# Kernel optimization log

Hardware: AMD Instinct MI355X
Metric: run time of the kernel (lower is better)

The kernel has to match this reference:

```python
import jax, jax.numpy as jnp
import numpy as np

H = 4          # no_heads
C_HIDDEN = 32  # per-head hidden dim


def setup_inputs() -> dict:
    key = jax.random.key(0)
    ks = jax.random.split(key, 11)
    B, S, C = 1, 256, 128
    sc = 1.0 / np.sqrt(C).astype(np.float32)
    return {
        "q_x": jax.random.normal(ks[0], (B, S, S, C), jnp.float32),
        "kv_x": jax.random.normal(ks[1], (B, S, S, C), jnp.float32),
        "bias1": jax.random.normal(ks[2], (B, 1, H, S, S), jnp.float32),
        "bias2": jax.random.normal(ks[3], (B, S, 1, 1, S), jnp.float32),
        "wq": jax.random.normal(ks[4], (C, C), jnp.float32) * sc,
        "wk": jax.random.normal(ks[5], (C, C), jnp.float32) * sc,
        "wv": jax.random.normal(ks[6], (C, C), jnp.float32) * sc,
        "wg": jax.random.normal(ks[7], (C, C), jnp.float32) * sc,
        "bg": jax.random.normal(ks[8], (C,), jnp.float32) * 0.02,
        "wo": jax.random.normal(ks[9], (C, C), jnp.float32) * sc,
        "bo": jax.random.normal(ks[10], (C,), jnp.float32) * 0.02,
    }


def reference(q_x, kv_x, bias1, bias2, wq, wk, wv, wg, bg, wo, bo):
    # Linear projections (torch Linear semantics: x @ W^T), no bias on q/k/v.
    def split_heads(x):  # ... Q (H C) -> ... H Q C
        *lead, Q, _ = x.shape
        return jnp.moveaxis(x.reshape(*lead, Q, H, C_HIDDEN), -2, -3)

    q = split_heads(jnp.einsum('...qi,oi->...qo', q_x, wq)) / np.sqrt(C_HIDDEN)
    k = split_heads(jnp.einsum('...ki,oi->...ko', kv_x, wk))
    v = split_heads(jnp.einsum('...ki,oi->...ko', kv_x, wv))

    # scores: [B, S, H, Q, K]
    a = jnp.einsum('bshqd,bshkd->bshqk', q, k)
    a = a + bias1 + bias2
    a = jax.nn.softmax(a, axis=-1)
    o = jnp.einsum('bshqk,bshkd->bshqd', a, v)
    o = jnp.moveaxis(o, -3, -2)  # ... H Q C -> ... Q H C

    # sigmoid gating
    g = jax.nn.sigmoid(jnp.einsum('...qi,oi->...qo', q_x, wg) + bg)
    *lead, Q, _ = g.shape
    g = g.reshape(*lead, Q, H, C_HIDDEN)
    o = o * g

    o = o.reshape(*lead, Q, H * C_HIDDEN)
    return jnp.einsum('...qi,oi->...qo', o, wo) + bo
```

## Files before the change

kernel.cpp:

```cpp
#include <hip/hip_runtime.h>
#include <math.h>

typedef _Float16 f16;
typedef _Float16 h4 __attribute__((ext_vector_type(4)));
typedef _Float16 h8 __attribute__((ext_vector_type(8)));
typedef float f32x4 __attribute__((ext_vector_type(4)));

#define QSCALE 0.17677669529663689f

__global__ __launch_bounds__(256) void proj_mfma(
    const float* __restrict__ q_x, const float* __restrict__ kv_x,
    const float* __restrict__ wq, const float* __restrict__ wk,
    const float* __restrict__ wv, const float* __restrict__ wg,
    const float* __restrict__ bg,
    f16* __restrict__ qb, f16* __restrict__ kb,
    f16* __restrict__ vbT, f16* __restrict__ gb)
{
    __shared__ char lds[65536];
    char* xl = lds;
    char* wl = lds + 32768;
    const int t = threadIdx.x;
    const int lane = t & 63, wave = t >> 6;
    const int wr = wave >> 1, wc = wave & 1;
    const int lo = lane & 15, hi = lane >> 4;
    const int phase = blockIdx.y;
    const int row0 = blockIdx.x * 128;
    const float* xsrc = phase ? kv_x : q_x;

    #pragma unroll
    for (int j = 0; j < 16; ++j) {
        int f = t + 256 * j;
        int row = f >> 5, c4 = f & 31;
        float4 v = *(const float4*)(xsrc + (size_t)(row0 + row) * 128 + c4 * 4);
        h4 hv = {(f16)v.x, (f16)v.y, (f16)v.z, (f16)v.w};
        *(h4*)(xl + row * 256 + (((c4 >> 1) ^ (row & 7)) << 4) + ((c4 & 1) << 3)) = hv;
    }

    for (int sub = 0; sub < 2; ++sub) {
        const int pid = phase * 2 + sub;
        const float* w = (pid == 0) ? wq : (pid == 1) ? wg : (pid == 2) ? wk : wv;
        __syncthreads();
        #pragma unroll
        for (int j = 0; j < 16; ++j) {
            int f = t + 256 * j;
            int row = f >> 5, c4 = f & 31;
            float4 v = *(const float4*)(w + (size_t)row * 128 + c4 * 4);
            h4 hv = {(f16)v.x, (f16)v.y, (f16)v.z, (f16)v.w};
            *(h4*)(wl + row * 256 + (((c4 >> 1) ^ (row & 7)) << 4) + ((c4 & 1) << 3)) = hv;
        }
        __syncthreads();

        f32x4 acc[4][4];
        #pragma unroll
        for (int m = 0; m < 4; ++m)
            #pragma unroll
            for (int n = 0; n < 4; ++n) acc[m][n] = (f32x4){0.f, 0.f, 0.f, 0.f};

        #pragma unroll
        for (int kk = 0; kk < 4; ++kk) {
            const int swz = ((hi + 4 * kk) ^ (lo & 7)) << 4;
            h8 af[4], bf[4];
            #pragma unroll
            for (int m = 0; m < 4; ++m)
                af[m] = *(const h8*)(xl + (lo + 16 * m + 64 * wr) * 256 + swz);
            #pragma unroll
            for (int n = 0; n < 4; ++n)
                bf[n] = *(const h8*)(wl + (lo + 16 * n + 64 * wc) * 256 + swz);
            #pragma unroll
            for (int m = 0; m < 4; ++m)
                #pragma unroll
                for (int n = 0; n < 4; ++n)
                    acc[m][n] = __builtin_amdgcn_mfma_f32_16x16x32_f16(af[m], bf[n], acc[m][n], 0, 0, 0);
        }

        #pragma unroll
        for (int n = 0; n < 4; ++n) {
            const int col = 64 * wc + 16 * n + lo;
            const float bgv = (pid == 1) ? bg[col] : 0.f;
            #pragma unroll
            for (int m = 0; m < 4; ++m) {
                if (pid == 3) {
                    int rg = row0 + 64 * wr + 16 * m + 4 * hi;
                    int sidx = rg >> 8, key = rg & 255;
                    int hh = col >> 5, dh = col & 31;
                    h4 hv = {(f16)acc[m][n][0], (f16)acc[m][n][1],
                             (f16)acc[m][n][2], (f16)acc[m][n][3]};
                    *(h4*)(vbT + (((size_t)sidx * 4 + hh) * 32 + dh) * 256 + key) = hv;
                } else {
                    f16* dst = (pid == 0) ? qb : (pid == 1) ? gb : kb;
                    #pragma unroll
                    for (int r = 0; r < 4; ++r) {
                        int rg = row0 + 64 * wr + 16 * m + 4 * hi + r;
                        float v = acc[m][n][r];
                        if (pid == 0) v *= QSCALE;
                        else if (pid == 1) v = 1.f / (1.f + __expf(-(v + bgv)));
                        dst[(size_t)rg * 128 + col] = (f16)v;
                    }
                }
            }
        }
    }
}

__global__ __launch_bounds__(256) void attn_mfma(
    const f16* __restrict__ qb, const f16* __restrict__ kb,
    const f16* __restrict__ vbT, const f16* __restrict__ gb,
    const float* __restrict__ bias1, const float* __restrict__ bias2,
    f16* __restrict__ ob)
{
    __shared__ float b2s[256];
    __shared__ char plds[32768];
    const int x = blockIdx.x;
    const int h = x >> 2, qblk = x & 3;
    const int s = blockIdx.y;
    const int t = threadIdx.x, wave = t >> 6, lane = t & 63;
    const int lo = lane & 15, hi = lane >> 4;
    char* pw = plds + wave * 8192;
    const size_t rowbase = (size_t)s * 256;
    const int q0 = qblk * 64 + wave * 16;

    b2s[t] = bias2[s * 256 + t];
    __syncthreads();

    h8 qf = *(const h8*)(qb + (rowbase + q0 + lo) * 128 + h * 32 + 8 * hi);

    const float* b1 = bias1 + (size_t)h * 65536;
    f32x4 acc[16];
    #pragma unroll
    for (int nt = 0; nt < 16; ++nt) {
        float b2v = b2s[16 * nt + lo];
        #pragma unroll
        for (int r = 0; r < 4; ++r)
            acc[nt][r] = b1[(q0 + 4 * hi + r) * 256 + 16 * nt + lo] + b2v;
    }
    #pragma unroll
    for (int nt = 0; nt < 16; ++nt) {
        h8 kf = *(const h8*)(kb + (rowbase + 16 * nt + lo) * 128 + h * 32 + 8 * hi);
        acc[nt] = __builtin_amdgcn_mfma_f32_16x16x32_f16(qf, kf, acc[nt], 0, 0, 0);
    }

    float inv_l[4];
    #pragma unroll
    for (int r = 0; r < 4; ++r) {
        float mx = acc[0][r];
        #pragma unroll
        for (int nt = 1; nt < 16; ++nt) mx = fmaxf(mx, acc[nt][r]);
        #pragma unroll
        for (int w = 1; w < 16; w <<= 1) mx = fmaxf(mx, __shfl_xor(mx, w, 16));
        float sm = 0.f;
        #pragma unroll
        for (int nt = 0; nt < 16; ++nt) {
            float p = __expf(acc[nt][r] - mx);
            acc[nt][r] = p;
            sm += p;
        }
        #pragma unroll
        for (int w = 1; w < 16; w <<= 1) sm += __shfl_xor(sm, w, 16);
        inv_l[r] = 1.f / sm;
    }

    #pragma unroll
    for (int nt = 0; nt < 16; ++nt)
        #pragma unroll
        for (int r = 0; r < 4; ++r) {
            int row = 4 * hi + r, k = 16 * nt + lo;
            int cs = (k >> 3) ^ (row & 7);
            *(f16*)(pw + row * 512 + cs * 16 + (k & 7) * 2) = (f16)acc[nt][r];
        }

    const f16* vbase = vbT + ((size_t)s * 4 + h) * 32 * 256;
    f32x4 Oa[2];
    Oa[0] = (f32x4){0.f, 0.f, 0.f, 0.f};
    Oa[1] = (f32x4){0.f, 0.f, 0.f, 0.f};
    #pragma unroll
    for (int kt = 0; kt < 8; ++kt) {
        int cs = (4 * kt + hi) ^ (lo & 7);
        h8 pa = *(const h8*)(pw + lo * 512 + cs * 16);
        #pragma unroll
        for (int n2 = 0; n2 < 2; ++n2) {
            h8 vf = *(const h8*)(vbase + (size_t)(n2 * 16 + lo) * 256 + 32 * kt + 8 * hi);
            Oa[n2] = __builtin_amdgcn_mfma_f32_16x16x32_f16(pa, vf, Oa[n2], 0, 0, 0);
        }
    }

    #pragma unroll
    for (int n2 = 0; n2 < 2; ++n2)
        #pragma unroll
        for (int r = 0; r < 4; ++r) {
            size_t idx = (rowbase + q0 + 4 * hi + r) * 128 + h * 32 + n2 * 16 + lo;
            float g = (float)gb[idx];
            ob[idx] = (f16)(Oa[n2][r] * inv_l[r] * g);
        }
}

__global__ __launch_bounds__(256) void out_mfma(
    const f16* __restrict__ ob, const float* __restrict__ wo,
    const float* __restrict__ bo, float* __restrict__ out)
{
    __shared__ char lds[65536];
    char* xl = lds;
    char* wl = lds + 32768;
    const int t = threadIdx.x;
    const int lane = t & 63, wave = t >> 6;
    const int wr = wave >> 1, wc = wave & 1;
    const int lo = lane & 15, hi = lane >> 4;
    const int row0 = blockIdx.x * 128;

    #pragma unroll
    for (int j = 0; j < 8; ++j) {
        int f = t + 256 * j;
        int row = f >> 4, c8 = f & 15;
        h8 v = *(const h8*)(ob + (size_t)(row0 + row) * 128 + c8 * 8);
        *(h8*)(xl + row * 256 + ((c8 ^ (row & 7)) << 4)) = v;
    }
    #pragma unroll
    for (int j = 0; j < 16; ++j) {
        int f = t + 256 * j;
        int row = f >> 5, c4 = f & 31;
        float4 v = *(const float4*)(wo + (size_t)row * 128 + c4 * 4);
        h4 hv = {(f16)v.x, (f16)v.y, (f16)v.z, (f16)v.w};
        *(h4*)(wl + row * 256 + (((c4 >> 1) ^ (row & 7)) << 4) + ((c4 & 1) << 3)) = hv;
    }
    __syncthreads();

    f32x4 acc[4][4];
    #pragma unroll
    for (int m = 0; m < 4; ++m)
        #pragma unroll
        for (int n = 0; n < 4; ++n) acc[m][n] = (f32x4){0.f, 0.f, 0.f, 0.f};

    #pragma unroll
    for (int kk = 0; kk < 4; ++kk) {
        const int swz = ((hi + 4 * kk) ^ (lo & 7)) << 4;
        h8 af[4], bf[4];
        #pragma unroll
        for (int m = 0; m < 4; ++m)
            af[m] = *(const h8*)(xl + (lo + 16 * m + 64 * wr) * 256 + swz);
        #pragma unroll
        for (int n = 0; n < 4; ++n)
            bf[n] = *(const h8*)(wl + (lo + 16 * n + 64 * wc) * 256 + swz);
        #pragma unroll
        for (int m = 0; m < 4; ++m)
            #pragma unroll
            for (int n = 0; n < 4; ++n)
                acc[m][n] = __builtin_amdgcn_mfma_f32_16x16x32_f16(af[m], bf[n], acc[m][n], 0, 0, 0);
    }

    #pragma unroll
    for (int n = 0; n < 4; ++n) {
        const int col = 64 * wc + 16 * n + lo;
        const float bov = bo[col];
        #pragma unroll
        for (int m = 0; m < 4; ++m)
            #pragma unroll
            for (int r = 0; r < 4; ++r)
                out[(size_t)(row0 + 64 * wr + 16 * m + 4 * hi + r) * 128 + col] = acc[m][n][r] + bov;
    }
}

extern "C" void kernel_launch(void* const* d_in, const int* in_sizes, int n_in,
                              void* d_out, int out_size, void* d_ws, size_t ws_size,
                              hipStream_t stream)
{
    const float* q_x   = (const float*)d_in[0];
    const float* kv_x  = (const float*)d_in[1];
    const float* bias1 = (const float*)d_in[2];
    const float* bias2 = (const float*)d_in[3];
    const float* wq    = (const float*)d_in[4];
    const float* wk    = (const float*)d_in[5];
    const float* wv    = (const float*)d_in[6];
    const float* wg    = (const float*)d_in[7];
    const float* bg    = (const float*)d_in[8];
    const float* wo    = (const float*)d_in[9];
    const float* bo    = (const float*)d_in[10];
    float* out = (float*)d_out;

    const size_t RC = (size_t)65536 * 128;
    f16* ws  = (f16*)d_ws;
    f16* qb  = ws;
    f16* kb  = ws + RC;
    f16* vbT = ws + 2 * RC;
    f16* gb  = ws + 3 * RC;
    f16* ob  = ws + 4 * RC;

    proj_mfma<<<dim3(512, 2), 256, 0, stream>>>(q_x, kv_x, wq, wk, wv, wg, bg, qb, kb, vbT, gb);
    attn_mfma<<<dim3(16, 256), 256, 0, stream>>>(qb, kb, vbT, gb, bias1, bias2, ob);
    out_mfma<<<512, 256, 0, stream>>>(ob, wo, bo, out);
}
```

Before: 157.4 us.

## Rewrite attention with 32x32 MFMA transposed scores and register-resident P

The attention kernel now computes transposed score tiles with 32x32x16 MFMA so each lane owns a full query row. Softmax then needs only a single cross-half shuffle, and the probability fragment is built in registers via lane swaps instead of a round trip through LDS. Each block now handles one (s, head) pair over two 128-query passes, with vectorized bias and gate loads. The 128 accumulator floats per lane raise register pressure, which the launch bound of 2 blocks per CU caps, and fewer, larger blocks change how the grid fills the device.

```diff
diff --git a/kernel.cpp b/kernel.cpp
--- a/kernel.cpp
+++ b/kernel.cpp
@@ -5,6 +5,10 @@
 typedef _Float16 h4 __attribute__((ext_vector_type(4)));
 typedef _Float16 h8 __attribute__((ext_vector_type(8)));
 typedef float f32x4 __attribute__((ext_vector_type(4)));
+typedef float f32x16 __attribute__((ext_vector_type(16)));
+typedef unsigned int u32;
+typedef u32 u32x2 __attribute__((ext_vector_type(2)));
+typedef u32 u32x4 __attribute__((ext_vector_type(4)));
 
 #define QSCALE 0.17677669529663689f
 
@@ -102,95 +106,103 @@
     }
 }
 
-__global__ __launch_bounds__(256) void attn_mfma(
+__global__ __launch_bounds__(256, 2) void attn_mfma(
     const f16* __restrict__ qb, const f16* __restrict__ kb,
     const f16* __restrict__ vbT, const f16* __restrict__ gb,
     const float* __restrict__ bias1, const float* __restrict__ bias2,
     f16* __restrict__ ob)
 {
-    __shared__ float b2s[256];
-    __shared__ char plds[32768];
-    const int x = blockIdx.x;
-    const int h = x >> 2, qblk = x & 3;
-    const int s = blockIdx.y;
+    const int s = blockIdx.x, h = blockIdx.y;
     const int t = threadIdx.x, wave = t >> 6, lane = t & 63;
-    const int lo = lane & 15, hi = lane >> 4;
-    char* pw = plds + wave * 8192;
+    const int q32 = lane & 31;
+    const int b = lane >> 5;
     const size_t rowbase = (size_t)s * 256;
-    const int q0 = qblk * 64 + wave * 16;
-
-    b2s[t] = bias2[s * 256 + t];
-    __syncthreads();
-
-    h8 qf = *(const h8*)(qb + (rowbase + q0 + lo) * 128 + h * 32 + 8 * hi);
-
+    const f16* kslab = kb + rowbase * 128 + h * 32;
+    const f16* vslab = vbT + ((size_t)s * 4 + h) * 32 * 256;
     const float* b1 = bias1 + (size_t)h * 65536;
-    f32x4 acc[16];
-    #pragma unroll
-    for (int nt = 0; nt < 16; ++nt) {
-        float b2v = b2s[16 * nt + lo];
-        #pragma unroll
-        for (int r = 0; r < 4; ++r)
-            acc[nt][r] = b1[(q0 + 4 * hi + r) * 256 + 16 * nt + lo] + b2v;
-    }
-    #pragma unroll
-    for (int nt = 0; nt < 16; ++nt) {
-        h8 kf = *(const h8*)(kb + (rowbase + 16 * nt + lo) * 128 + h * 32 + 8 * hi);
-        acc[nt] = __builtin_amdgcn_mfma_f32_16x16x32_f16(qf, kf, acc[nt], 0, 0, 0);
-    }
-
-    float inv_l[4];
-    #pragma unroll
-    for (int r = 0; r < 4; ++r) {
-        float mx = acc[0][r];
-        #pragma unroll
-        for (int nt = 1; nt < 16; ++nt) mx = fmaxf(mx, acc[nt][r]);
-        #pragma unroll
-        for (int w = 1; w < 16; w <<= 1) mx = fmaxf(mx, __shfl_xor(mx, w, 16));
+    const float* b2 = bias2 + (size_t)s * 256;
+
+    for (int pass = 0; pass < 2; ++pass) {
+        const int q0 = pass * 128 + wave * 32;
+
+        h8 qf[2];
+        #pragma unroll
+        for (int dh = 0; dh < 2; ++dh)
+            qf[dh] = *(const h8*)(qb + (rowbase + q0 + q32) * 128 + h * 32 + 16 * dh + 8 * b);
+
+        f32x16 acc[8];
+        #pragma unroll
+        for (int ktt = 0; ktt < 8; ++ktt) {
+            #pragma unroll
+            for (int rq = 0; rq < 4; ++rq) {
+                f32x4 b1v = *(const f32x4*)(b1 + (size_t)(q0 + q32) * 256 + 32 * ktt + 8 * rq + 4 * b);
+                f32x4 b2v = *(const f32x4*)(b2 + 32 * ktt + 8 * rq + 4 * b);
+                #pragma unroll
+                for (int i = 0; i < 4; ++i) acc[ktt][4 * rq + i] = b1v[i] + b2v[i];
+            }
+            #pragma unroll
+            for (int dh = 0; dh < 2; ++dh) {
+                h8 kf = *(const h8*)(kslab + (size_t)(32 * ktt + q32) * 128 + 16 * dh + 8 * b);
+                acc[ktt] = __builtin_amdgcn_mfma_f32_32x32x16_f16(kf, qf[dh], acc[ktt], 0, 0, 0);
+            }
+        }
+
+        float mx = acc[0][0];
+        #pragma unroll
+        for (int ktt = 0; ktt < 8; ++ktt)
+            #pragma unroll
+            for (int i = 0; i < 16; ++i) mx = fmaxf(mx, acc[ktt][i]);
+        mx = fmaxf(mx, __shfl_xor(mx, 32));
         float sm = 0.f;
         #pragma unroll
-        for (int nt = 0; nt < 16; ++nt) {
-            float p = __expf(acc[nt][r] - mx);
-            acc[nt][r] = p;
-            sm += p;
-        }
-        #pragma unroll
-        for (int w = 1; w < 16; w <<= 1) sm += __shfl_xor(sm, w, 16);
-        inv_l[r] = 1.f / sm;
-    }
-
-    #pragma unroll
-    for (int nt = 0; nt < 16; ++nt)
-        #pragma unroll
-        for (int r = 0; r < 4; ++r) {
-            int row = 4 * hi + r, k = 16 * nt + lo;
-            int cs = (k >> 3) ^ (row & 7);
-            *(f16*)(pw + row * 512 + cs * 16 + (k & 7) * 2) = (f16)acc[nt][r];
-        }
-
-    const f16* vbase = vbT + ((size_t)s * 4 + h) * 32 * 256;
-    f32x4 Oa[2];
-    Oa[0] = (f32x4){0.f, 0.f, 0.f, 0.f};
-    Oa[1] = (f32x4){0.f, 0.f, 0.f, 0.f};
-    #pragma unroll
-    for (int kt = 0; kt < 8; ++kt) {
-        int cs = (4 * kt + hi) ^ (lo & 7);
-        h8 pa = *(const h8*)(pw + lo * 512 + cs * 16);
-        #pragma unroll
-        for (int n2 = 0; n2 < 2; ++n2) {
-            h8 vf = *(const h8*)(vbase + (size_t)(n2 * 16 + lo) * 256 + 32 * kt + 8 * hi);
-            Oa[n2] = __builtin_amdgcn_mfma_f32_16x16x32_f16(pa, vf, Oa[n2], 0, 0, 0);
-        }
-    }
-
-    #pragma unroll
-    for (int n2 = 0; n2 < 2; ++n2)
-        #pragma unroll
-        for (int r = 0; r < 4; ++r) {
-            size_t idx = (rowbase + q0 + 4 * hi + r) * 128 + h * 32 + n2 * 16 + lo;
-            float g = (float)gb[idx];
-            ob[idx] = (f16)(Oa[n2][r] * inv_l[r] * g);
-        }
+        for (int ktt = 0; ktt < 8; ++ktt)
+            #pragma unroll
+            for (int i = 0; i < 16; ++i) {
+                float p = __expf(acc[ktt][i] - mx);
+                acc[ktt][i] = p;
+                sm += p;
+            }
+        sm += __shfl_xor(sm, 32);
+        const float inv_l = 1.f / sm;
+
+        f32x16 O;
+        #pragma unroll
+        for (int i = 0; i < 16; ++i) O[i] = 0.f;
+
+        #pragma unroll
+        for (int kt = 0; kt < 16; ++kt) {
+            const int e = 8 * (kt & 1);
+            const f32x16& a = acc[kt >> 1];
+            h4 lowh  = {(f16)a[e + 0], (f16)a[e + 1], (f16)a[e + 2], (f16)a[e + 3]};
+            h4 highh = {(f16)a[e + 4], (f16)a[e + 5], (f16)a[e + 6], (f16)a[e + 7]};
+            u32x2 low  = __builtin_bit_cast(u32x2, lowh);
+            u32x2 high = __builtin_bit_cast(u32x2, highh);
+            u32x2 swl, swh;
+            swl.x = (u32)__shfl_xor((int)low.x, 32);
+            swl.y = (u32)__shfl_xor((int)low.y, 32);
+            swh.x = (u32)__shfl_xor((int)high.x, 32);
+            swh.y = (u32)__shfl_xor((int)high.y, 32);
+            u32x4 wfr;
+            wfr.x = b ? swh.x : low.x;
+            wfr.y = b ? swh.y : low.y;
+            wfr.z = b ? high.x : swl.x;
+            wfr.w = b ? high.y : swl.y;
+            h8 pfrag = __builtin_bit_cast(h8, wfr);
+            h8 vf = *(const h8*)(vslab + (size_t)q32 * 256 + 16 * kt + 8 * b);
+            O = __builtin_amdgcn_mfma_f32_32x32x16_f16(vf, pfrag, O, 0, 0, 0);
+        }
+
+        #pragma unroll
+        for (int rq = 0; rq < 4; ++rq) {
+            size_t idx = (rowbase + q0 + q32) * 128 + h * 32 + 8 * rq + 4 * b;
+            h4 g4 = *(const h4*)(gb + idx);
+            h4 o4;
+            #pragma unroll
+            for (int i = 0; i < 4; ++i)
+                o4[i] = (f16)(O[4 * rq + i] * inv_l * (float)g4[i]);
+            *(h4*)(ob + idx) = o4;
+        }
+    }
 }
 
 __global__ __launch_bounds__(256) void out_mfma(
@@ -284,6 +296,6 @@
     f16* ob  = ws + 4 * RC;
 
     proj_mfma<<<dim3(512, 2), 256, 0, stream>>>(q_x, kv_x, wq, wk, wv, wg, bg, qb, kb, vbT, gb);
-    attn_mfma<<<dim3(16, 256), 256, 0, stream>>>(qb, kb, vbT, gb, bias1, bias2, ob);
+    attn_mfma<<<dim3(256, 4), 256, 0, stream>>>(qb, kb, vbT, gb, bias1, bias2, ob);
     out_mfma<<<512, 256, 0, stream>>>(ob, wo, bo, out);
 }
```

Measured after the change: 186.8 us. +18.7%, slower.

## Restructure attention to one block per (row, head) with K/V staged in LDS

Applied to the files above, without the earlier changes.

The attention kernel now assigns one block per sequence row and head, staging that head's K and V slabs into shared memory once and having each wave process 32 queries across two passes. Scores are computed in two 128-key chunks with an online softmax (running max and sum rescaling). This replaces the earlier design, where four blocks per head each reread K and V from global memory. The trade-offs are 64KB of dynamic LDS per block, which limits occupancy, a grid cut to 1024 blocks, and the extra rescaling arithmetic.

```diff
diff --git a/kernel.cpp b/kernel.cpp
--- a/kernel.cpp
+++ b/kernel.cpp
@@ -102,95 +102,155 @@
     }
 }
 
-__global__ __launch_bounds__(256) void attn_mfma(
+__global__ __launch_bounds__(256, 2) void attn_mfma(
     const f16* __restrict__ qb, const f16* __restrict__ kb,
     const f16* __restrict__ vbT, const f16* __restrict__ gb,
     const float* __restrict__ bias1, const float* __restrict__ bias2,
     f16* __restrict__ ob)
 {
-    __shared__ float b2s[256];
-    __shared__ char plds[32768];
-    const int x = blockIdx.x;
-    const int h = x >> 2, qblk = x & 3;
-    const int s = blockIdx.y;
+    extern __shared__ char smem[];
+    char* klds = smem;
+    char* vlds = smem + 16384;
+    char* plds = smem + 32768;
+    const int s = blockIdx.x, h = blockIdx.y;
     const int t = threadIdx.x, wave = t >> 6, lane = t & 63;
     const int lo = lane & 15, hi = lane >> 4;
     char* pw = plds + wave * 8192;
     const size_t rowbase = (size_t)s * 256;
-    const int q0 = qblk * 64 + wave * 16;
-
-    b2s[t] = bias2[s * 256 + t];
+    const f16* kslab = kb + rowbase * 128 + h * 32;
+    const f16* vslab = vbT + ((size_t)s * 4 + h) * 32 * 256;
+    const float* b1 = bias1 + (size_t)h * 65536;
+    const float* b2 = bias2 + (size_t)s * 256;
+
+    #pragma unroll
+    for (int it = 0; it < 4; ++it) {
+        int idx = t + 256 * it;
+        int key = idx >> 2, c = idx & 3;
+        h8 v = *(const h8*)(kslab + (size_t)key * 128 + c * 8);
+        *(h8*)(klds + ((key >> 5) * 4 + c) * 512 + (key & 31) * 16) = v;
+    }
+    #pragma unroll
+    for (int it = 0; it < 4; ++it) {
+        int idx = t + 256 * it;
+        int d = idx & 31, kc = idx >> 5;
+        h8 v = *(const h8*)(vslab + (size_t)d * 256 + kc * 8);
+        *(h8*)(vlds + kc * 512 + d * 16) = v;
+    }
     __syncthreads();
 
-    h8 qf = *(const h8*)(qb + (rowbase + q0 + lo) * 128 + h * 32 + 8 * hi);
-
-    const float* b1 = bias1 + (size_t)h * 65536;
-    f32x4 acc[16];
-    #pragma unroll
-    for (int nt = 0; nt < 16; ++nt) {
-        float b2v = b2s[16 * nt + lo];
-        #pragma unroll
-        for (int r = 0; r < 4; ++r)
-            acc[nt][r] = b1[(q0 + 4 * hi + r) * 256 + 16 * nt + lo] + b2v;
-    }
-    #pragma unroll
-    for (int nt = 0; nt < 16; ++nt) {
-        h8 kf = *(const h8*)(kb + (rowbase + 16 * nt + lo) * 128 + h * 32 + 8 * hi);
-        acc[nt] = __builtin_amdgcn_mfma_f32_16x16x32_f16(qf, kf, acc[nt], 0, 0, 0);
-    }
-
-    float inv_l[4];
-    #pragma unroll
-    for (int r = 0; r < 4; ++r) {
-        float mx = acc[0][r];
-        #pragma unroll
-        for (int nt = 1; nt < 16; ++nt) mx = fmaxf(mx, acc[nt][r]);
-        #pragma unroll
-        for (int w = 1; w < 16; w <<= 1) mx = fmaxf(mx, __shfl_xor(mx, w, 16));
-        float sm = 0.f;
-        #pragma unroll
-        for (int nt = 0; nt < 16; ++nt) {
-            float p = __expf(acc[nt][r] - mx);
-            acc[nt][r] = p;
-            sm += p;
-        }
-        #pragma unroll
-        for (int w = 1; w < 16; w <<= 1) sm += __shfl_xor(sm, w, 16);
-        inv_l[r] = 1.f / sm;
-    }
-
-    #pragma unroll
-    for (int nt = 0; nt < 16; ++nt)
-        #pragma unroll
-        for (int r = 0; r < 4; ++r) {
-            int row = 4 * hi + r, k = 16 * nt + lo;
-            int cs = (k >> 3) ^ (row & 7);
-            *(f16*)(pw + row * 512 + cs * 16 + (k & 7) * 2) = (f16)acc[nt][r];
-        }
-
-    const f16* vbase = vbT + ((size_t)s * 4 + h) * 32 * 256;
-    f32x4 Oa[2];
-    Oa[0] = (f32x4){0.f, 0.f, 0.f, 0.f};
-    Oa[1] = (f32x4){0.f, 0.f, 0.f, 0.f};
-    #pragma unroll
-    for (int kt = 0; kt < 8; ++kt) {
-        int cs = (4 * kt + hi) ^ (lo & 7);
-        h8 pa = *(const h8*)(pw + lo * 512 + cs * 16);
-        #pragma unroll
-        for (int n2 = 0; n2 < 2; ++n2) {
-            h8 vf = *(const h8*)(vbase + (size_t)(n2 * 16 + lo) * 256 + 32 * kt + 8 * hi);
-            Oa[n2] = __builtin_amdgcn_mfma_f32_16x16x32_f16(pa, vf, Oa[n2], 0, 0, 0);
-        }
-    }
-
-    #pragma unroll
-    for (int n2 = 0; n2 < 2; ++n2)
-        #pragma unroll
-        for (int r = 0; r < 4; ++r) {
-            size_t idx = (rowbase + q0 + 4 * hi + r) * 128 + h * 32 + n2 * 16 + lo;
-            float g = (float)gb[idx];
-            ob[idx] = (f16)(Oa[n2][r] * inv_l[r] * g);
-        }
+    for (int pass = 0; pass < 2; ++pass) {
+        const int q0 = pass * 128 + wave * 32;
+
+        h8 qf[2];
+        #pragma unroll
+        for (int m = 0; m < 2; ++m)
+            qf[m] = *(const h8*)(qb + (rowbase + q0 + 16 * m + lo) * 128 + h * 32 + 8 * hi);
+
+        f32x4 O[2][2];
+        float mrun[2][4], lrun[2][4];
+        #pragma unroll
+        for (int m = 0; m < 2; ++m) {
+            #pragma unroll
+            for (int n2 = 0; n2 < 2; ++n2) O[m][n2] = (f32x4){0.f, 0.f, 0.f, 0.f};
+            #pragma unroll
+            for (int r = 0; r < 4; ++r) { mrun[m][r] = -1e30f; lrun[m][r] = 0.f; }
+        }
+
+        #pragma unroll
+        for (int ch = 0; ch < 2; ++ch) {
+            f32x4 acc[2][8];
+            #pragma unroll
+            for (int m = 0; m < 2; ++m)
+                #pragma unroll
+                for (int nt = 0; nt < 8; ++nt) {
+                    const float b2v = b2[ch * 128 + 16 * nt + lo];
+                    #pragma unroll
+                    for (int r = 0; r < 4; ++r)
+                        acc[m][nt][r] = b1[(size_t)(q0 + 16 * m + 4 * hi + r) * 256
+                                           + ch * 128 + 16 * nt + lo] + b2v;
+                }
+            #pragma unroll
+            for (int nt = 0; nt < 8; ++nt) {
+                const int ntg = ch * 8 + nt;
+                h8 kf = *(const h8*)(klds + ((ntg >> 1) * 4 + hi) * 512
+                                     + ((ntg & 1) * 16 + lo) * 16);
+                #pragma unroll
+                for (int m = 0; m < 2; ++m)
+                    acc[m][nt] = __builtin_amdgcn_mfma_f32_16x16x32_f16(qf[m], kf, acc[m][nt], 0, 0, 0);
+            }
+
+            float scale[2][4];
+            #pragma unroll
+            for (int m = 0; m < 2; ++m)
+                #pragma unroll
+                for (int r = 0; r < 4; ++r) {
+                    float mx = acc[m][0][r];
+                    #pragma unroll
+                    for (int nt = 1; nt < 8; ++nt) mx = fmaxf(mx, acc[m][nt][r]);
+                    #pragma unroll
+                    for (int w = 1; w < 16; w <<= 1) mx = fmaxf(mx, __shfl_xor(mx, w, 16));
+                    const float mn = fmaxf(mrun[m][r], mx);
+                    scale[m][r] = __expf(mrun[m][r] - mn);
+                    mrun[m][r] = mn;
+                    float sm = 0.f;
+                    #pragma unroll
+                    for (int nt = 0; nt < 8; ++nt) {
+                        float p = __expf(acc[m][nt][r] - mn);
+                        acc[m][nt][r] = p;
+                        sm += p;
+                    }
+                    #pragma unroll
+                    for (int w = 1; w < 16; w <<= 1) sm += __shfl_xor(sm, w, 16);
+                    lrun[m][r] = lrun[m][r] * scale[m][r] + sm;
+                }
+            #pragma unroll
+            for (int m = 0; m < 2; ++m)
+                #pragma unroll
+                for (int n2 = 0; n2 < 2; ++n2)
+                    #pragma unroll
+                    for (int r = 0; r < 4; ++r) O[m][n2][r] *= scale[m][r];
+
+            #pragma unroll
+            for (int m = 0; m < 2; ++m)
+                #pragma unroll
+                for (int nt = 0; nt < 8; ++nt)
+                    #pragma unroll
+                    for (int r = 0; r < 4; ++r) {
+                        const int row = 16 * m + 4 * hi + r;
+                        const int cs = ((2 * nt + (lo >> 3)) ^ ((4 * m + hi) << 1)) & 15;
+                        *(f16*)(pw + row * 256 + cs * 16 + (lo & 7) * 2) = (f16)acc[m][nt][r];
+                    }
+
+            #pragma unroll
+            for (int kt = 0; kt < 4; ++kt) {
+                #pragma unroll
+                for (int m = 0; m < 2; ++m) {
+                    const int row = 16 * m + lo;
+                    const int cs = ((4 * kt + hi) ^ ((4 * m + (lo >> 2)) << 1)) & 15;
+                    h8 pa = *(const h8*)(pw + row * 256 + cs * 16);
+                    #pragma unroll
+                    for (int n2 = 0; n2 < 2; ++n2) {
+                        h8 vf = *(const h8*)(vlds + (ch * 16 + 4 * kt + hi) * 512
+                                             + (16 * n2 + lo) * 16);
+                        O[m][n2] = __builtin_amdgcn_mfma_f32_16x16x32_f16(pa, vf, O[m][n2], 0, 0, 0);
+                    }
+                }
+            }
+        }
+
+        #pragma unroll
+        for (int m = 0; m < 2; ++m)
+            #pragma unroll
+            for (int r = 0; r < 4; ++r) {
+                const float inv = 1.f / lrun[m][r];
+                #pragma unroll
+                for (int n2 = 0; n2 < 2; ++n2) {
+                    size_t idx = (rowbase + q0 + 16 * m + 4 * hi + r) * 128
+                                 + h * 32 + 16 * n2 + lo;
+                    ob[idx] = (f16)(O[m][n2][r] * inv * (float)gb[idx]);
+                }
+            }
+    }
 }
 
 __global__ __launch_bounds__(256) void out_mfma(
@@ -284,6 +344,6 @@
     f16* ob  = ws + 4 * RC;
 
     proj_mfma<<<dim3(512, 2), 256, 0, stream>>>(q_x, kv_x, wq, wk, wv, wg, bg, qb, kb, vbT, gb);
-    attn_mfma<<<dim3(16, 256), 256, 0, stream>>>(qb, kb, vbT, gb, bias1, bias2, ob);
+    attn_mfma<<<dim3(256, 4), 256, 65536, stream>>>(qb, kb, vbT, gb, bias1, bias2, ob);
     out_mfma<<<512, 256, 0, stream>>>(ob, wo, bo, out);
 }
```

Result: faster. 139.7 us (-11.2%).
